# Kernel tuning notes

Hardware: AMD Instinct MI355X
Metric: run time of the kernel (lower is better)

## Reference

```python
import jax, jax.numpy as jnp
import numpy as np
from jax import lax

N = 262144      # number of samples
C = 256         # number of classes
N_BINS = 15     # default n_bins
P = 2           # default p


def setup_inputs() -> dict:
    key = jax.random.key(0)
    k1, k2 = jax.random.split(key)
    return {
        "logits_target": jax.random.normal(k1, (N, C), dtype=jnp.float32),
        "labels_target": jax.random.randint(k2, (N,), 0, C, dtype=jnp.int32),
    }


def _per_class_ece(conf, lab_f):
    """conf: [N] float confidences for one class; lab_f: [N] float {0,1} labels.
    Adaptive equal-count bins, version='our' leave-one-out calibration stat."""
    n = conf.shape[0]
    conf_c = lax.stop_gradient(conf)  # torch computes edges on detached cpu copy
    sorted_conf = jnp.sort(conf_c)
    # histedges_equalN: np.interp(linspace(0, n, n_bins+1), arange(n), sort(x))
    edges = jnp.interp(
        jnp.linspace(0.0, float(n), N_BINS + 1),
        jnp.arange(n, dtype=conf.dtype),
        sorted_conf,
    )  # [N_BINS+1]
    # in_bin for bin k: conf > edges[k] and conf <= edges[k+1]
    # searchsorted(side='left') gives smallest i with edges[i] >= conf -> bin = i-1
    bin_id = jnp.searchsorted(edges, conf_c, side="left") - 1  # [N]
    valid = bin_id >= 0  # conf == min boundary falls in no bin (strict lower bound)
    seg = jnp.where(valid, bin_id, N_BINS)  # dump invalid into extra segment
    sum_lab = jax.ops.segment_sum(lab_f, seg, num_segments=N_BINS + 1)
    cnt = jax.ops.segment_sum(jnp.ones_like(lab_f), seg, num_segments=N_BINS + 1)
    # leave-one-out conditional expectation per element
    cond_exp = (sum_lab[seg] - lab_f) / (cnt[seg] - 1.0)
    contrib = jnp.where(valid, jnp.abs(conf - cond_exp) ** P, 0.0)
    return contrib.sum() / n


def reference(logits_target, labels_target):
    probs = jax.nn.softmax(logits_target, axis=1)  # [N, C]
    # one-hot-style per-class binary labels, [C, N]
    lab = (labels_target[None, :] == jnp.arange(C, dtype=labels_target.dtype)[:, None]).astype(probs.dtype)
    per_class_ce = jax.vmap(_per_class_ece)(probs.T, lab)  # [C]
    return per_class_ce
```

## Files before the change

kernel.cpp:

```cpp
#include <hip/hip_runtime.h>
#include <hip/hip_bf16.h>

#define NROWS 262144
#define NC 256
#define NB 15

typedef float f32x4 __attribute__((ext_vector_type(4)));

#define NH 5048
#define NHP 5120

#define WS_FAST_TOTAL 134217728ull

__device__ __forceinline__ int key_bits(unsigned int b)
{
    unsigned int e = b >> 23;
    int k;
    if (e < 115u)       k = (int)(b >> 20);
    else if (e <= 122u) k = (int)(b >> 14) - 57960;
    else { k = (int)(b >> 20) + 4032; if (k > NH - 1) k = NH - 1; }
    return k;
}

__device__ __forceinline__ float lo_val(int k)
{
    unsigned int b;
    if (k < 920)       b = (unsigned int)k << 20;
    else if (k < 5016) b = (unsigned int)(k + 57960) << 14;
    else               b = (unsigned int)(k - 4032) << 20;
    return __uint_as_float(b);
}

__device__ __forceinline__ unsigned int pack_bf16(float a, float b)
{
    unsigned int ua = __float_as_uint(a);
    unsigned int ub = __float_as_uint(b);
    ua += 0x7FFFu + ((ua >> 16) & 1u);
    ub += 0x7FFFu + ((ub >> 16) & 1u);
    return (ua >> 16) | (ub & 0xFFFF0000u);
}

__device__ __forceinline__ float wave_sum_dpp(float x)
{
    int v = __float_as_int(x);
#define DPP_ADD(ctrl, rmask) do {                                              \
        int s_ = __builtin_amdgcn_update_dpp(0, v, ctrl, rmask, 0xf, true);    \
        v = __float_as_int(__int_as_float(v) + __int_as_float(s_));            \
    } while (0)
    DPP_ADD(0x111, 0xf);
    DPP_ADD(0x112, 0xf);
    DPP_ADD(0x114, 0xf);
    DPP_ADD(0x118, 0xf);
    DPP_ADD(0x142, 0xa);
    DPP_ADD(0x143, 0xc);
#undef DPP_ADD
    return __int_as_float(__builtin_amdgcn_readlane(v, 63));
}

extern "C" __global__ __launch_bounds__(512)
void k_transpose(const float* __restrict__ logits,
                 unsigned short* __restrict__ probsT16)
{
    __shared__ unsigned int tileP[32 * 264];
    const int t = threadIdx.x;
    const int lane = t & 63;
    const int w = t >> 6;
    const int rowBase = blockIdx.x * 64;

    f32x4 va[4], vb[4];
    #pragma unroll
    for (int p = 0; p < 4; ++p) {
        const int ra = rowBase + w * 8 + 2 * p;
        va[p] = __builtin_nontemporal_load((const f32x4*)(logits + (size_t)ra * NC) + lane);
        vb[p] = __builtin_nontemporal_load((const f32x4*)(logits + (size_t)(ra + 1) * NC) + lane);
    }

    #pragma unroll
    for (int p = 0; p < 4; ++p) {
        float a0 = __expf(va[p].x - 8.0f), a1 = __expf(va[p].y - 8.0f);
        float a2 = __expf(va[p].z - 8.0f), a3 = __expf(va[p].w - 8.0f);
        float b0 = __expf(vb[p].x - 8.0f), b1 = __expf(vb[p].y - 8.0f);
        float b2 = __expf(vb[p].z - 8.0f), b3 = __expf(vb[p].w - 8.0f);
        float sa = wave_sum_dpp((a0 + a1) + (a2 + a3));
        float sb = wave_sum_dpp((b0 + b1) + (b2 + b3));
        float ia = 1.0f / sa, ib = 1.0f / sb;
        unsigned int d0 = pack_bf16(a0 * ia, b0 * ib);
        unsigned int d1 = pack_bf16(a1 * ia, b1 * ib);
        unsigned int d2 = pack_bf16(a2 * ia, b2 * ib);
        unsigned int d3 = pack_bf16(a3 * ia, b3 * ib);
        *(uint4*)(&tileP[(w * 4 + p) * 264 + lane * 4]) = make_uint4(d0, d1, d2, d3);
    }
    __syncthreads();

    {
        const int cls = t >> 1, h = t & 1;
        unsigned int v[16];
        #pragma unroll
        for (int j = 0; j < 16; ++j) v[j] = tileP[(h * 16 + j) * 264 + cls];
        uint4* dst = (uint4*)(probsT16 + (size_t)blockIdx.x * 16384 + cls * 64 + h * 32);
        dst[0] = make_uint4(v[0],  v[1],  v[2],  v[3]);
        dst[1] = make_uint4(v[4],  v[5],  v[6],  v[7]);
        dst[2] = make_uint4(v[8],  v[9],  v[10], v[11]);
        dst[3] = make_uint4(v[12], v[13], v[14], v[15]);
    }
}

extern "C" __global__ __launch_bounds__(1024)
void k_class(const unsigned short* __restrict__ probsT16, const int* __restrict__ labels,
             float* __restrict__ out)
{
    __shared__ unsigned int hist[NHP];
    __shared__ float wpart[16];
    __shared__ int edgB[16];
    __shared__ float lab1[48];
    __shared__ float red[16][48];
    __shared__ float Fred[48];
    __shared__ double dbin[NB];

    const int c = blockIdx.x;
    const int t = threadIdx.x;
    const int lane = t & 63;
    const int w = t >> 6;

    for (int i = t; i < NHP; i += 1024) hist[i] = 0u;
    if (t < 48) lab1[t] = 0.0f;
    __syncthreads();

#define PB(bits) atomicAdd(&hist[key_bits(bits)], 1u)
#define PB4(v) do { PB((v).x << 16); PB((v).x & 0xFFFF0000u); \
                    PB((v).y << 16); PB((v).y & 0xFFFF0000u); \
                    PB((v).z << 16); PB((v).z & 0xFFFF0000u); \
                    PB((v).w << 16); PB((v).w & 0xFFFF0000u); } while (0)
    {
        const int sub = t & 7;
        const int ch0 = t >> 3;
        const unsigned short* base = probsT16 + (size_t)c * 64;
        #pragma unroll 1
        for (int i = 0; i < 32; i += 4) {
            const size_t g0 = (size_t)(i * 128 + ch0) * 16384;
            uint4 v0 = *((const uint4*)(base + g0)            + sub);
            uint4 v1 = *((const uint4*)(base + g0 + 2097152)  + sub);
            uint4 v2 = *((const uint4*)(base + g0 + 4194304)  + sub);
            uint4 v3 = *((const uint4*)(base + g0 + 6291456)  + sub);
            PB4(v0); PB4(v1); PB4(v2); PB4(v3);
        }
    }
#undef PB4
#undef PB
    __syncthreads();

    const int k0 = t * 5;
    float ms[5], sx[5], sq[5];
    {
        float lo = lo_val(k0);
        #pragma unroll
        for (int u = 0; u < 5; ++u) {
            float hi = lo_val(k0 + u + 1);
            float n = (float)hist[k0 + u];
            float ctr = 0.5f * (lo + hi);
            ms[u] = n; sx[u] = n * ctr; sq[u] = n * ctr * ctr;
            lo = hi;
        }
    }
    float mysum = ms[0] + ms[1] + ms[2] + ms[3] + ms[4];

    float inc = mysum;
    #pragma unroll
    for (int d = 1; d < 64; d <<= 1) {
        float v = __shfl_up(inc, d);
        if (lane >= d) inc += v;
    }
    if (lane == 63) wpart[w] = inc;
    __syncthreads();
    if (t == 0) {
        float run = 0.0f;
        #pragma unroll
        for (int i = 0; i < 16; ++i) { float x = wpart[i]; wpart[i] = run; run += x; }
    }
    __syncthreads();
    float base = wpart[w] + inc - mysum;

    float cums[5];
    cums[0] = base;
    #pragma unroll
    for (int u = 1; u < 5; ++u) cums[u] = cums[u - 1] + ms[u - 1];

    #pragma unroll
    for (int j = 1; j <= 14; ++j) {
        float q = (float)j * (262144.0f / 15.0f);
        #pragma unroll
        for (int u = 0; u < 5; ++u) {
            int k = k0 + u;
            if (ms[u] > 0.0f && cums[u] <= q && q < cums[u] + ms[u])
                edgB[j] = (q - cums[u] > 0.5f * ms[u]) ? (k + 1) : k;
        }
    }
    __syncthreads();

    int Bj[15];
    Bj[0] = 0;
    #pragma unroll
    for (int j = 1; j <= 14; ++j) Bj[j] = edgB[j];

    float F1[15], Fx[15], Fq[15];
    #pragma unroll
    for (int j = 0; j < 15; ++j) { F1[j] = 0.0f; Fx[j] = 0.0f; Fq[j] = 0.0f; }

    #pragma unroll
    for (int u = 0; u < 5; ++u) {
        int k = k0 + u;
        #pragma unroll
        for (int j = 0; j < 15; ++j) {
            if (k >= Bj[j]) { F1[j] += ms[u]; Fx[j] += sx[u]; Fq[j] += sq[u]; }
        }
    }

    #pragma unroll
    for (int j = 0; j < 15; ++j) {
        #pragma unroll
        for (int off = 32; off; off >>= 1) {
            F1[j] += __shfl_xor(F1[j], off);
            Fx[j] += __shfl_xor(Fx[j], off);
            Fq[j] += __shfl_xor(Fq[j], off);
        }
    }
    if (lane == 0) {
        #pragma unroll
        for (int j = 0; j < 15; ++j) {
            red[w][j] = F1[j];
            red[w][15 + j] = Fx[j];
            red[w][30 + j] = Fq[j];
        }
    }

    {
        const uint4* lab4 = (const uint4*)labels;
        const unsigned int cc = (unsigned int)c;
        uint4 L = lab4[t];
        #pragma unroll 1
        for (int i = t; i < NROWS / 4; i += 1024) {
            uint4 Ln;
            if (i + 1024 < NROWS / 4) Ln = lab4[i + 1024];
            if (L.x == cc || L.y == cc || L.z == cc || L.w == cc) {
                #pragma unroll
                for (int e = 0; e < 4; ++e) {
                    unsigned int lv = (e == 0) ? L.x : (e == 1) ? L.y : (e == 2) ? L.z : L.w;
                    if (lv == cc) {
                        int r = 4 * i + e;
                        unsigned int bits =
                            (unsigned int)probsT16[(size_t)(r >> 6) * 16384 + c * 64 + (r & 63)] << 16;
                        float x = __uint_as_float(bits);
                        int key = key_bits(bits);
                        int bin = 0;
                        #pragma unroll
                        for (int j = 1; j <= 14; ++j) bin += (key >= Bj[j]) ? 1 : 0;
                        atomicAdd(&lab1[bin * 3 + 0], 1.0f);
                        atomicAdd(&lab1[bin * 3 + 1], x);
                        atomicAdd(&lab1[bin * 3 + 2], x * x);
                    }
                }
            }
            L = Ln;
        }
    }
    __syncthreads();

    if (t < 45) {
        float s = 0.0f;
        #pragma unroll
        for (int i = 0; i < 16; ++i) s += red[i][t];
        Fred[t] = s;
    }
    __syncthreads();

    if (t < NB) {
        const int b = t;
        double n  = (double)(Fred[b]      - ((b < NB - 1) ? Fred[b + 1]      : 0.0f));
        double T  = (double)(Fred[15 + b] - ((b < NB - 1) ? Fred[15 + b + 1] : 0.0f));
        double Q  = (double)(Fred[30 + b] - ((b < NB - 1) ? Fred[30 + b + 1] : 0.0f));
        double n1 = (double)lab1[b * 3 + 0];
        double T1 = (double)lab1[b * 3 + 1];
        double Q1 = (double)lab1[b * 3 + 2];
        double contrib = 0.0;
        if (n >= 2.0) {
            double d = n - 1.0;
            double mu0 = n1 / d;
            double mu1 = (n1 - 1.0) / d;
            double n0 = n - n1, T0 = T - T1, Q0 = Q - Q1;
            contrib = (Q0 - 2.0 * mu0 * T0 + n0 * mu0 * mu0)
                    + (Q1 - 2.0 * mu1 * T1 + n1 * mu1 * mu1);
        }
        dbin[b] = contrib;
    }
    __syncthreads();
    if (t == 0) {
        double V = 0.0;
        for (int b = 0; b < NB; ++b) V += dbin[b];
        out[c] = (float)(V / (double)NROWS);
    }
}

#define FB_HBITS 15
#define FB_HSIZE (1 << FB_HBITS)
#define FB_HSHIFT (32 - FB_HBITS)
#define FB_EDGES_OFF  33554432u
#define FB_STATS_OFF  33570816u
#define FB_TOTAL      (33570816u + 92160u)

extern "C" __global__ __launch_bounds__(256)
void fb_softmax_hist(const float* __restrict__ logits, unsigned int* __restrict__ hist)
{
    const int lane = threadIdx.x & 63;
    const int nwaves = (gridDim.x * blockDim.x) >> 6;
    const int gwave = (blockIdx.x * blockDim.x + threadIdx.x) >> 6;
    for (int row = gwave; row < NROWS; row += nwaves) {
        float4 v = ((const float4*)(logits + (size_t)row * NC))[lane];
        float m = fmaxf(fmaxf(v.x, v.y), fmaxf(v.z, v.w));
        for (int off = 32; off; off >>= 1) m = fmaxf(m, __shfl_xor(m, off));
        float e0 = __expf(v.x - m), e1 = __expf(v.y - m);
        float e2 = __expf(v.z - m), e3 = __expf(v.w - m);
        float s = e0 + e1 + e2 + e3;
        for (int off = 32; off; off >>= 1) s += __shfl_xor(s, off);
        float inv = 1.0f / s;
        int cls = lane * 4;
        atomicAdd(&hist[(size_t)(cls + 0) * FB_HSIZE + (__float_as_uint(e0 * inv) >> FB_HSHIFT)], 1u);
        atomicAdd(&hist[(size_t)(cls + 1) * FB_HSIZE + (__float_as_uint(e1 * inv) >> FB_HSHIFT)], 1u);
        atomicAdd(&hist[(size_t)(cls + 2) * FB_HSIZE + (__float_as_uint(e2 * inv) >> FB_HSHIFT)], 1u);
        atomicAdd(&hist[(size_t)(cls + 3) * FB_HSIZE + (__float_as_uint(e3 * inv) >> FB_HSHIFT)], 1u);
    }
}

extern "C" __global__ __launch_bounds__(256)
void fb_edges(const unsigned int* __restrict__ hist, float* __restrict__ edges)
{
    __shared__ unsigned int pref[256];
    const int c = blockIdx.x;
    const unsigned int* h = hist + (size_t)c * FB_HSIZE;
    const int t = threadIdx.x;
    const int CH = FB_HSIZE / 256;
    unsigned int sum = 0;
    for (int i = 0; i < CH; ++i) sum += h[t * CH + i];
    pref[t] = sum;
    __syncthreads();
    if (t == 0) {
        unsigned int run = 0;
        for (int i = 0; i < 256; ++i) { unsigned int x = pref[i]; pref[i] = run; run += x; }
    }
    __syncthreads();
    if (t < 16) {
        double q = (double)t * (double)NROWS / 15.0;
        if (q > (double)(NROWS - 1)) q = (double)(NROWS - 1);
        int lo = 0;
        for (int i = 1; i < 256; ++i) if ((double)pref[i] <= q) lo = i;
        double cum = (double)pref[lo];
        int b = lo * CH;
        unsigned int m = 0;
        for (int i = 0; i < CH; ++i, ++b) {
            m = h[b];
            if (m && cum + (double)m > q) break;
            cum += (double)m;
        }
        double f = (q - cum) / (double)m;
        float flo = __uint_as_float(((unsigned int)b) << FB_HSHIFT);
        float fhi = __uint_as_float(((unsigned int)(b + 1)) << FB_HSHIFT);
        edges[c * 16 + t] = (float)((double)flo + f * ((double)fhi - (double)flo));
    }
}

extern "C" __global__ __launch_bounds__(1024)
void fb_stats(const float* __restrict__ logits, const int* __restrict__ labels,
              const float* __restrict__ edges, float* __restrict__ stats)
{
    __shared__ float acc[NC * NB * 2 * 3];
    for (int i = threadIdx.x; i < NC * NB * 6; i += blockDim.x) acc[i] = 0.0f;
    const int lane = threadIdx.x & 63;
    const int wave = threadIdx.x >> 6;
    const int cls0 = lane * 4;
    float4 E[4][4];
    #pragma unroll
    for (int j = 0; j < 4; ++j) {
        const float4* ep = (const float4*)(edges + (size_t)(cls0 + j) * 16);
        E[j][0] = ep[0]; E[j][1] = ep[1]; E[j][2] = ep[2]; E[j][3] = ep[3];
    }
    __syncthreads();
    const int rowsPer = NROWS / 256;
    const int rowBase = blockIdx.x * rowsPer;
    for (int r = wave; r < rowsPer; r += 16) {
        const int row = rowBase + r;
        float4 v = ((const float4*)(logits + (size_t)row * NC))[lane];
        float m = fmaxf(fmaxf(v.x, v.y), fmaxf(v.z, v.w));
        for (int off = 32; off; off >>= 1) m = fmaxf(m, __shfl_xor(m, off));
        float e0 = __expf(v.x - m), e1 = __expf(v.y - m);
        float e2 = __expf(v.z - m), e3 = __expf(v.w - m);
        float s = e0 + e1 + e2 + e3;
        for (int off = 32; off; off >>= 1) s += __shfl_xor(s, off);
        float inv = 1.0f / s;
        float cf[4] = { e0 * inv, e1 * inv, e2 * inv, e3 * inv };
        const int lab_cls = labels[row];
        #pragma unroll
        for (int j = 0; j < 4; ++j) {
            float x = cf[j];
            int cnt = 0;
            #pragma unroll
            for (int kk = 0; kk < 4; ++kk) {
                cnt += (E[j][kk].x < x); cnt += (E[j][kk].y < x);
                cnt += (E[j][kk].z < x); cnt += (E[j][kk].w < x);
            }
            int bin = cnt - 1;
            if (bin < 0) continue;
            if (bin > NB - 1) bin = NB - 1;
            int lab = (lab_cls == (cls0 + j)) ? 1 : 0;
            int base = (((cls0 + j) * NB + bin) * 2 + lab) * 3;
            atomicAdd(&acc[base + 0], 1.0f);
            atomicAdd(&acc[base + 1], x);
            atomicAdd(&acc[base + 2], x * x);
        }
    }
    __syncthreads();
    for (int i = threadIdx.x; i < NC * NB * 6; i += blockDim.x) {
        float a = acc[i];
        if (a != 0.0f) atomicAdd(&stats[i], a);
    }
}

extern "C" __global__ __launch_bounds__(256)
void fb_final(const float* __restrict__ stats, float* __restrict__ out)
{
    const int c = threadIdx.x;
    double total = 0.0;
    for (int b = 0; b < NB; ++b) {
        const float* p = stats + ((size_t)(c * NB + b) * 2) * 3;
        double n0 = p[0], T0 = p[1], Q0 = p[2];
        double n1 = p[3], T1 = p[4], Q1 = p[5];
        double ct = n0 + n1;
        if (ct == 0.0) continue;
        double d = ct - 1.0;
        double mu0 = n1 / d;
        double mu1 = (n1 - 1.0) / d;
        total += Q0 - 2.0 * mu0 * T0 + n0 * mu0 * mu0;
        total += Q1 - 2.0 * mu1 * T1 + n1 * mu1 * mu1;
    }
    out[c] = (float)(total / (double)NROWS);
}

extern "C" void kernel_launch(void* const* d_in, const int* in_sizes, int n_in,
                              void* d_out, int out_size, void* d_ws, size_t ws_size,
                              hipStream_t stream)
{
    const float* logits = (const float*)d_in[0];
    const int* labels = (const int*)d_in[1];
    float* out = (float*)d_out;
    unsigned char* ws = (unsigned char*)d_ws;

    if (ws_size >= WS_FAST_TOTAL) {
        unsigned short* probsT16 = (unsigned short*)ws;

        hipLaunchKernelGGL(k_transpose, dim3(NROWS / 64), dim3(512), 0, stream,
                           logits, probsT16);
        hipLaunchKernelGGL(k_class, dim3(NC), dim3(1024), 0, stream,
                           probsT16, labels, out);
    } else {
        unsigned int* hist = (unsigned int*)ws;
        float* edges = (float*)(ws + FB_EDGES_OFF);
        float* stats = (float*)(ws + FB_STATS_OFF);
        hipMemsetAsync(ws, 0, FB_TOTAL, stream);
        hipLaunchKernelGGL(fb_softmax_hist, dim3(1024), dim3(256), 0, stream, logits, hist);
        hipLaunchKernelGGL(fb_edges, dim3(NC), dim3(256), 0, stream, hist, edges);
        hipLaunchKernelGGL(fb_stats, dim3(256), dim3(1024), 0, stream, logits, labels, edges, stats);
        hipLaunchKernelGGL(fb_final, dim3(1), dim3(256), 0, stream, stats, out);
    }
}
```

Before: 177.9 us.

## Use 8-row class-major chunks to drop the LDS transpose in softmax kernel

The intermediate bf16 probability layout changes from 64-row blocks per class to 8-row chunks per class (16 bytes per class per chunk). Each wave can then write its 8 rows straight from registers, which removes the shared-memory tile, the barrier, and the transposed LDS reads from k_transpose, and the block shrinks to 256 threads. The histogram and label-lookup reads in k_class are re-indexed to match. In exchange, each k_class thread now reads 16-byte pieces spaced 4 KB apart rather than 128-byte contiguous runs, which may cost memory-access efficiency.

```diff
diff --git a/kernel.cpp b/kernel.cpp
--- a/kernel.cpp
+++ b/kernel.cpp
@@ -57,24 +57,24 @@
     return __int_as_float(__builtin_amdgcn_readlane(v, 63));
 }
 
-extern "C" __global__ __launch_bounds__(512)
+extern "C" __global__ __launch_bounds__(256)
 void k_transpose(const float* __restrict__ logits,
                  unsigned short* __restrict__ probsT16)
 {
-    __shared__ unsigned int tileP[32 * 264];
     const int t = threadIdx.x;
     const int lane = t & 63;
     const int w = t >> 6;
-    const int rowBase = blockIdx.x * 64;
+    const int rowBase = blockIdx.x * 32 + w * 8;
 
     f32x4 va[4], vb[4];
     #pragma unroll
     for (int p = 0; p < 4; ++p) {
-        const int ra = rowBase + w * 8 + 2 * p;
+        const int ra = rowBase + 2 * p;
         va[p] = __builtin_nontemporal_load((const f32x4*)(logits + (size_t)ra * NC) + lane);
         vb[p] = __builtin_nontemporal_load((const f32x4*)(logits + (size_t)(ra + 1) * NC) + lane);
     }
 
+    unsigned int o0[4], o1[4], o2[4], o3[4];
     #pragma unroll
     for (int p = 0; p < 4; ++p) {
         float a0 = __expf(va[p].x - 8.0f), a1 = __expf(va[p].y - 8.0f);
@@ -84,24 +84,19 @@
         float sa = wave_sum_dpp((a0 + a1) + (a2 + a3));
         float sb = wave_sum_dpp((b0 + b1) + (b2 + b3));
         float ia = 1.0f / sa, ib = 1.0f / sb;
-        unsigned int d0 = pack_bf16(a0 * ia, b0 * ib);
-        unsigned int d1 = pack_bf16(a1 * ia, b1 * ib);
-        unsigned int d2 = pack_bf16(a2 * ia, b2 * ib);
-        unsigned int d3 = pack_bf16(a3 * ia, b3 * ib);
-        *(uint4*)(&tileP[(w * 4 + p) * 264 + lane * 4]) = make_uint4(d0, d1, d2, d3);
-    }
-    __syncthreads();
+        o0[p] = pack_bf16(a0 * ia, b0 * ib);
+        o1[p] = pack_bf16(a1 * ia, b1 * ib);
+        o2[p] = pack_bf16(a2 * ia, b2 * ib);
+        o3[p] = pack_bf16(a3 * ia, b3 * ib);
+    }
 
     {
-        const int cls = t >> 1, h = t & 1;
-        unsigned int v[16];
-        #pragma unroll
-        for (int j = 0; j < 16; ++j) v[j] = tileP[(h * 16 + j) * 264 + cls];
-        uint4* dst = (uint4*)(probsT16 + (size_t)blockIdx.x * 16384 + cls * 64 + h * 32);
-        dst[0] = make_uint4(v[0],  v[1],  v[2],  v[3]);
-        dst[1] = make_uint4(v[4],  v[5],  v[6],  v[7]);
-        dst[2] = make_uint4(v[8],  v[9],  v[10], v[11]);
-        dst[3] = make_uint4(v[12], v[13], v[14], v[15]);
+        const size_t g = (size_t)(rowBase >> 3);
+        unsigned int* base = (unsigned int*)(probsT16 + g * 2048) + lane * 16;
+        *(uint4*)(base + 0)  = make_uint4(o0[0], o0[1], o0[2], o0[3]);
+        *(uint4*)(base + 4)  = make_uint4(o1[0], o1[1], o1[2], o1[3]);
+        *(uint4*)(base + 8)  = make_uint4(o2[0], o2[1], o2[2], o2[3]);
+        *(uint4*)(base + 12) = make_uint4(o3[0], o3[1], o3[2], o3[3]);
     }
 }
 
@@ -132,16 +127,14 @@
                     PB((v).z << 16); PB((v).z & 0xFFFF0000u); \
                     PB((v).w << 16); PB((v).w & 0xFFFF0000u); } while (0)
     {
-        const int sub = t & 7;
-        const int ch0 = t >> 3;
-        const unsigned short* base = probsT16 + (size_t)c * 64;
+        const unsigned short* base = probsT16 + (size_t)c * 8;
         #pragma unroll 1
-        for (int i = 0; i < 32; i += 4) {
-            const size_t g0 = (size_t)(i * 128 + ch0) * 16384;
-            uint4 v0 = *((const uint4*)(base + g0)            + sub);
-            uint4 v1 = *((const uint4*)(base + g0 + 2097152)  + sub);
-            uint4 v2 = *((const uint4*)(base + g0 + 4194304)  + sub);
-            uint4 v3 = *((const uint4*)(base + g0 + 6291456)  + sub);
+        for (int i = 0; i < 8; ++i) {
+            const size_t ch = (size_t)i * 4096 + t;
+            uint4 v0 = *(const uint4*)(base + (ch         ) * 2048);
+            uint4 v1 = *(const uint4*)(base + (ch + 1024  ) * 2048);
+            uint4 v2 = *(const uint4*)(base + (ch + 2048  ) * 2048);
+            uint4 v3 = *(const uint4*)(base + (ch + 3072  ) * 2048);
             PB4(v0); PB4(v1); PB4(v2); PB4(v3);
         }
     }
@@ -248,7 +241,7 @@
                     if (lv == cc) {
                         int r = 4 * i + e;
                         unsigned int bits =
-                            (unsigned int)probsT16[(size_t)(r >> 6) * 16384 + c * 64 + (r & 63)] << 16;
+                            (unsigned int)probsT16[(size_t)(r >> 3) * 2048 + c * 8 + (r & 7)] << 16;
                         float x = __uint_as_float(bits);
                         int key = key_bits(bits);
                         int bin = 0;
@@ -455,7 +448,7 @@
     if (ws_size >= WS_FAST_TOTAL) {
         unsigned short* probsT16 = (unsigned short*)ws;
 
-        hipLaunchKernelGGL(k_transpose, dim3(NROWS / 64), dim3(512), 0, stream,
+        hipLaunchKernelGGL(k_transpose, dim3(NROWS / 32), dim3(256), 0, stream,
                            logits, probsT16);
         hipLaunchKernelGGL(k_class, dim3(NC), dim3(1024), 0, stream,
                            probsT16, labels, out);
```

Measured after the change: 304.7 us. 71.3% more time.
